# Kernel optimization log

Hardware: AMD Instinct MI355X
Metric: run time of the kernel (lower is better)

The kernel has to match this reference:

```python
import jax, jax.numpy as jnp
import numpy as np

D_MODEL = 1024
NUM_HEADS = 16
HEAD_DIM = D_MODEL // NUM_HEADS  # used only for score scaling, as in the torch code


def setup_inputs() -> dict:
    key = jax.random.key(0)
    ks = jax.random.split(key, 8)
    B, S, D = 4, 2048, D_MODEL
    w_scale = 1.0 / np.sqrt(D)
    return {
        "x": jax.random.normal(ks[0], (B, S, D), dtype=jnp.float32),
        "Wq": jax.random.normal(ks[1], (D, D), dtype=jnp.float32) * w_scale,
        "bq": jnp.zeros((D,), dtype=jnp.float32),
        "Wk": jax.random.normal(ks[2], (D, D), dtype=jnp.float32) * w_scale,
        "bk": jnp.zeros((D,), dtype=jnp.float32),
        "Wv": jax.random.normal(ks[3], (D, D), dtype=jnp.float32) * w_scale,
        "bv": jnp.zeros((D,), dtype=jnp.float32),
        "temperature_scale": jnp.ones((1,), dtype=jnp.float32),
    }


def reference(x, Wq, bq, Wk, bk, Wv, bv, temperature_scale):
    # q, k, v: (B, S, D) -- no head split in the original module
    q = x @ Wq + bq
    k = x @ Wk + bk
    v = x @ Wv + bv
    scale = jnp.asarray(HEAD_DIM, x.dtype) ** 0.5
    # scores: (B, S, S)
    scores = jnp.einsum("bqd,bkd->bqk", q, k) / scale / temperature_scale[0]
    probs = jax.nn.softmax(scores, axis=-1)
    # per-row attention entropy (B, S, 1)
    entropy = -jnp.sum(probs * jnp.log(probs + 1e-8), axis=-1, keepdims=True)
    attention_output = jnp.einsum("bqk,bkd->bqd", probs, v)
    return attention_output, entropy.mean()
```

## Files before the change

kernel.cpp:

```cpp
#include <hip/hip_runtime.h>
#include <hip/hip_bf16.h>
#include <cstdint>
#include <cstddef>


typedef __attribute__((ext_vector_type(8))) short short8;
typedef __attribute__((ext_vector_type(4))) short short4v;
typedef __attribute__((ext_vector_type(4))) float f32x4;

#define GLOBAL_AS __attribute__((address_space(1)))
#define LDS_AS __attribute__((address_space(3)))

__device__ __forceinline__ void async_load16(const void* g, void* lds) {
  __builtin_amdgcn_global_load_lds((GLOBAL_AS void*)g, (LDS_AS void*)lds, 16, 0, 0);
}

__device__ __forceinline__ short f2bf_s(float x) {
  __hip_bfloat16 h = __float2bfloat16(x);
  return *reinterpret_cast<short*>(&h);
}

template <int MODE>
__device__ __forceinline__
void gemm_body(const __hip_bfloat16* __restrict__ A,
               const __hip_bfloat16* __restrict__ Bt,
               void* __restrict__ Cout,
               const float* __restrict__ bias,
               int K, int lda, int ldb, int ldc,
               __hip_bfloat16* __restrict__ sA,
               __hip_bfloat16* __restrict__ sB,
               int m0, int n0,
               const float* __restrict__ aux) {
  const int tid  = threadIdx.x;
  const int lane = tid & 63;
  const int wid  = tid >> 6;
  const int wm = (wid >> 1) * 64;
  const int wn = (wid & 1) * 64;
  const int quad = lane >> 4;
  const int rc   = lane & 15;

  f32x4 acc[4][4] = {};

  const int srow = tid >> 3;
  const int scol = ((tid & 7) ^ ((tid >> 3) & 7)) * 8;
  const __hip_bfloat16* Ag = A  + (size_t)(m0 + srow) * lda + scol;
  const __hip_bfloat16* Bg = Bt + (size_t)(n0 + srow) * ldb + scol;

  for (int k0 = 0; k0 < K; k0 += 64) {
#pragma unroll
    for (int p = 0; p < 4; ++p) {
      async_load16(Ag + k0 + (size_t)(32 * p) * lda, &sA[(wid * 64 + 256 * p) * 8]);
      async_load16(Bg + k0 + (size_t)(32 * p) * ldb, &sB[(wid * 64 + 256 * p) * 8]);
    }
    __syncthreads();

#pragma unroll
    for (int kk = 0; kk < 2; ++kk) {
      const int xo = ((kk * 4 + quad) ^ (rc & 7)) * 8;
      short8 af[4], bf[4];
#pragma unroll
      for (int i = 0; i < 4; ++i)
        af[i] = *(const short8*)&sA[(wm + i * 16 + rc) * 64 + xo];
#pragma unroll
      for (int i = 0; i < 4; ++i)
        bf[i] = *(const short8*)&sB[(wn + i * 16 + rc) * 64 + xo];

#pragma unroll
      for (int mi = 0; mi < 4; ++mi)
#pragma unroll
        for (int ni = 0; ni < 4; ++ni)
          acc[mi][ni] = __builtin_amdgcn_mfma_f32_16x16x32_bf16(
              af[mi], bf[ni], acc[mi][ni], 0, 0, 0);
    }
    __syncthreads();
  }

  if (MODE == 4) {
#pragma unroll
    for (int mi = 0; mi < 4; ++mi) {
      float sc[4];
#pragma unroll
      for (int r = 0; r < 4; ++r)
        sc[r] = aux[m0 + wm + mi * 16 + quad * 4 + r];
#pragma unroll
      for (int ni = 0; ni < 4; ++ni) {
        const int col = n0 + wn + ni * 16 + rc;
#pragma unroll
        for (int r = 0; r < 4; ++r) {
          const int row = m0 + wm + mi * 16 + quad * 4 + r;
          ((float*)Cout)[(size_t)row * ldc + col] = acc[mi][ni][r] * sc[r];
        }
      }
    }
  } else {
    const float qsc = (MODE == 1 && aux) ? 1.0f / (8.0f * aux[0]) : 1.0f;
#pragma unroll
    for (int mi = 0; mi < 4; ++mi) {
#pragma unroll
      for (int ni = 0; ni < 4; ++ni) {
        const int col = n0 + wn + ni * 16 + rc;
        const float badd = bias[col];
        if (MODE == 2) {
          const int rowb = m0 + wm + mi * 16 + quad * 4;
          short4v o;
#pragma unroll
          for (int r = 0; r < 4; ++r) o[r] = f2bf_s(acc[mi][ni][r] + badd);
          const size_t idx = (size_t)(rowb >> 11) * (1024u * 2048u) +
                             (size_t)col * 2048u + (size_t)(rowb & 2047);
          *(short4v*)((short*)Cout + idx) = o;
        } else {
#pragma unroll
          for (int r = 0; r < 4; ++r) {
            const int row = m0 + wm + mi * 16 + quad * 4 + r;
            ((__hip_bfloat16*)Cout)[(size_t)row * ldc + col] =
                __float2bfloat16((acc[mi][ni][r] + badd) * qsc);
          }
        }
      }
    }
  }
}

__global__ __launch_bounds__(256)
void qkv_fused(const __hip_bfloat16* __restrict__ xb,
               const __hip_bfloat16* __restrict__ Wt,
               __hip_bfloat16* __restrict__ qb, __hip_bfloat16* __restrict__ kb,
               __hip_bfloat16* __restrict__ vt,
               const float* __restrict__ bq, const float* __restrict__ bk,
               const float* __restrict__ bv, const float* __restrict__ tptr) {
  __shared__ __align__(16) __hip_bfloat16 sA[128 * 64];
  __shared__ __align__(16) __hip_bfloat16 sB[128 * 64];
  const int lin = blockIdx.x;
  const int j = lin & 7, t = lin >> 3;
  const int x = t & 7;
  const int G = j + 8 * (t >> 3);
  const int z = G >> 6, y = G & 63;
  const int m0 = y * 128, n0 = x * 128;

  const __hip_bfloat16* B = Wt + (size_t)z * 1024 * 1024;
  if (z == 0)
    gemm_body<1>(xb, B, qb, bq, 1024, 1024, 1024, 1024, sA, sB, m0, n0, tptr);
  else if (z == 1)
    gemm_body<1>(xb, B, kb, bk, 1024, 1024, 1024, 1024, sA, sB, m0, n0, nullptr);
  else
    gemm_body<2>(xb, B, vt, bv, 1024, 1024, 1024, 0, sA, sB, m0, n0, nullptr);
}

__global__ __launch_bounds__(512)
void scores_bigm(const __hip_bfloat16* __restrict__ qb,
                 const __hip_bfloat16* __restrict__ kb,
                 __hip_bfloat16* __restrict__ Pt,
                 float* __restrict__ stats) {
  __shared__ __align__(16) __hip_bfloat16 sA[256 * 64];
  __shared__ __align__(16) __hip_bfloat16 sB[128 * 64];
  const int lin = blockIdx.x;
  const int G = (lin & 7) * 64 + (lin >> 3);
  const size_t z = G >> 7;
  const int rr = G & 127;
  const int y = rr >> 4;
  const int x = rr & 15;
  const int m0 = y * 256, n0 = x * 128;
  const __hip_bfloat16* A  = qb + z * 2048 * 1024;
  const __hip_bfloat16* Bt = kb + z * 2048 * 1024;
  __hip_bfloat16* Cout = Pt + z * 2048 * 2048;
  float* st = stats + z * 2048 * 64;

  const int tid  = threadIdx.x;
  const int lane = tid & 63;
  const int wid  = tid >> 6;
  const int wm   = (wid >> 1) * 64;
  const int wn   = (wid & 1) * 64;
  const int quad = lane >> 4;
  const int rc   = lane & 15;

  f32x4 acc[4][4] = {};

  const int srow = tid >> 3;
  const int scol = ((tid & 7) ^ ((tid >> 3) & 7)) * 8;
  const __hip_bfloat16* Ag = A  + (size_t)(m0 + srow) * 1024 + scol;
  const __hip_bfloat16* Bg = Bt + (size_t)(n0 + srow) * 1024 + scol;

  for (int k0 = 0; k0 < 1024; k0 += 64) {
#pragma unroll
    for (int p = 0; p < 4; ++p)
      async_load16(Ag + k0 + (size_t)(64 * p) * 1024, &sA[(tid + 512 * p) * 8]);
#pragma unroll
    for (int p = 0; p < 2; ++p)
      async_load16(Bg + k0 + (size_t)(64 * p) * 1024, &sB[(tid + 512 * p) * 8]);
    __syncthreads();

#pragma unroll
    for (int kk = 0; kk < 2; ++kk) {
      const int xo = ((kk * 4 + quad) ^ (rc & 7)) * 8;
      short8 af[4], bf[4];
#pragma unroll
      for (int i = 0; i < 4; ++i)
        af[i] = *(const short8*)&sA[(wm + i * 16 + rc) * 64 + xo];
#pragma unroll
      for (int i = 0; i < 4; ++i)
        bf[i] = *(const short8*)&sB[(wn + i * 16 + rc) * 64 + xo];

#pragma unroll
      for (int mi = 0; mi < 4; ++mi)
#pragma unroll
        for (int ni = 0; ni < 4; ++ni)
          acc[mi][ni] = __builtin_amdgcn_mfma_f32_16x16x32_bf16(
              af[mi], bf[ni], acc[mi][ni], 0, 0, 0);
    }
    __syncthreads();
  }

  const int chunk = (n0 + wn) >> 6;
#pragma unroll
  for (int mi = 0; mi < 4; ++mi) {
    float l_acc[4] = {}, w_acc[4] = {};
#pragma unroll
    for (int ni = 0; ni < 4; ++ni)
#pragma unroll
      for (int r = 0; r < 4; ++r) {
        const float xv = acc[mi][ni][r];
        const float e = __expf(xv);
        acc[mi][ni][r] = e;
        l_acc[r] += e;
        w_acc[r] += e * xv;
      }
#pragma unroll
    for (int r = 0; r < 4; ++r) {
      float l = l_acc[r], w = w_acc[r];
#pragma unroll
      for (int off = 1; off < 16; off <<= 1) {
        l += __shfl_xor(l, off);
        w += __shfl_xor(w, off);
      }
      if (rc == 0) {
        const int row = m0 + wm + mi * 16 + quad * 4 + r;
        *(float2*)&st[((size_t)row * 32 + chunk) * 2] = make_float2(l, w);
      }
    }
#pragma unroll
    for (int ni = 0; ni < 4; ++ni) {
      const int col = n0 + wn + ni * 16 + rc;
#pragma unroll
      for (int r = 0; r < 4; ++r) {
        const int row = m0 + wm + mi * 16 + quad * 4 + r;
        Cout[(size_t)row * 2048 + col] = __float2bfloat16(acc[mi][ni][r]);
      }
    }
  }
}

__global__ __launch_bounds__(256)
void pv_swz(const __hip_bfloat16* __restrict__ Pt,
            const __hip_bfloat16* __restrict__ vt,
            float* __restrict__ out,
            const float* __restrict__ inv_l) {
  __shared__ __align__(16) __hip_bfloat16 sA[128 * 64];
  __shared__ __align__(16) __hip_bfloat16 sB[128 * 64];
  const int lin = blockIdx.x;
  const int j = lin & 7, t = lin >> 3;
  const int w = t & 3;
  const int G = j + 8 * (t >> 2);
  const size_t z = G >> 5;
  const int r = G & 31;
  const int y = (r >> 2) * 2 + (w >> 1);
  const int x = (r & 3) * 2 + (w & 1);
  gemm_body<4>(Pt + z * 2048 * 2048, vt + z * 1024 * 2048,
               out + z * 2048 * 1024, nullptr, 2048, 2048, 2048, 1024,
               sA, sB, y * 128, x * 128, inv_l + z * 2048);
}

__global__ __launch_bounds__(256)
void prep_fused(const float* __restrict__ x, __hip_bfloat16* __restrict__ xb,
                const float* __restrict__ Wq, const float* __restrict__ Wk,
                const float* __restrict__ Wv, __hip_bfloat16* __restrict__ Wt) {
  if (blockIdx.x < 4096) {
    const int i = (blockIdx.x * 256 + threadIdx.x) * 8;
    const float4 a = *(const float4*)(x + i);
    const float4 b = *(const float4*)(x + i + 4);
    short8 o;
    o[0] = f2bf_s(a.x); o[1] = f2bf_s(a.y); o[2] = f2bf_s(a.z); o[3] = f2bf_s(a.w);
    o[4] = f2bf_s(b.x); o[5] = f2bf_s(b.y); o[6] = f2bf_s(b.z); o[7] = f2bf_s(b.w);
    *(short8*)((short*)xb + i) = o;
  } else {
    __shared__ float tile[64][65];
    const int b = blockIdx.x - 4096;
    const int z = b >> 8;
    const int rem = b & 255;
    const int c0 = (rem & 15) * 64;
    const int r0 = (rem >> 4) * 64;
    const float* src = (z == 0) ? Wq : (z == 1) ? Wk : Wv;
    __hip_bfloat16* dst = Wt + (size_t)z * 1024 * 1024;
    const int lane = threadIdx.x & 63;
    const int grp  = threadIdx.x >> 6;
#pragma unroll
    for (int i = 0; i < 16; ++i) {
      const int r = grp * 16 + i;
      tile[r][lane] = src[(size_t)(r0 + r) * 1024 + c0 + lane];
    }
    __syncthreads();
#pragma unroll
    for (int i = 0; i < 16; ++i) {
      const int r = grp * 16 + i;
      dst[(size_t)(c0 + r) * 1024 + r0 + lane] = __float2bfloat16(tile[lane][r]);
    }
  }
}

__global__ __launch_bounds__(256)
void stats_reduce(const float* __restrict__ stats,
                  float* __restrict__ inv_l, float* __restrict__ Hrow) {
  const int row = blockIdx.x * 256 + threadIdx.x;
  const float* sp = stats + (size_t)row * 64;
  float l = 0.f, w = 0.f;
#pragma unroll
  for (int j = 0; j < 16; ++j) {
    const float4 a = *(const float4*)(sp + j * 4);
    l += a.x + a.z;
    w += a.y + a.w;
  }
  const float il = 1.0f / l;
  inv_l[row] = il;
  Hrow[row] = __logf(l) - w * il;
}

__global__ __launch_bounds__(256)
void reduce_entropy(const float* __restrict__ Hrow, float* __restrict__ out) {
  const int tid  = threadIdx.x;
  const int lane = tid & 63;
  const int wid  = tid >> 6;
  float s = 0.f;
#pragma unroll
  for (int j = 0; j < 8; ++j) {
    const float4 a = *(const float4*)(Hrow + j * 1024 + tid * 4);
    s += a.x + a.y + a.z + a.w;
  }
#pragma unroll
  for (int off = 1; off < 64; off <<= 1) s += __shfl_xor(s, off);
  __shared__ float red[4];
  if (lane == 0) red[wid] = s;
  __syncthreads();
  if (tid == 0)
    out[0] = (red[0] + red[1] + red[2] + red[3]) * (1.0f / 8192.0f);
}

extern "C" void kernel_launch(void* const* d_in, const int* in_sizes, int n_in,
                              void* d_out, int out_size, void* d_ws, size_t ws_size,
                              hipStream_t stream) {
  const float* x    = (const float*)d_in[0];
  const float* Wq   = (const float*)d_in[1];
  const float* bq   = (const float*)d_in[2];
  const float* Wk   = (const float*)d_in[3];
  const float* bk   = (const float*)d_in[4];
  const float* Wv   = (const float*)d_in[5];
  const float* bv   = (const float*)d_in[6];
  const float* temp = (const float*)d_in[7];
  float* out = (float*)d_out;
  char* ws = (char*)d_ws;

  __hip_bfloat16* qb    = (__hip_bfloat16*)(ws + 0);
  __hip_bfloat16* kb    = (__hip_bfloat16*)(ws + 16777216);
  __hip_bfloat16* vt    = (__hip_bfloat16*)(ws + 33554432);
  __hip_bfloat16* xb    = (__hip_bfloat16*)(ws + 50331648);
  __hip_bfloat16* Wt    = (__hip_bfloat16*)(ws + 67108864);
  __hip_bfloat16* Pt    = (__hip_bfloat16*)(ws + 73400320);
  float*          stats = (float*)(ws + 106954752);
  float*          inv_l = (float*)(ws + 109051904);
  float*          Hrow  = (float*)(ws + 109084672);

  prep_fused<<<4864, 256, 0, stream>>>(x, xb, Wq, Wk, Wv, Wt);

  qkv_fused<<<1536, 256, 0, stream>>>(xb, Wt, qb, kb, vt, bq, bk, bv, temp);

  scores_bigm<<<512, 512, 0, stream>>>(qb, kb, Pt, stats);
  stats_reduce<<<32, 256, 0, stream>>>(stats, inv_l, Hrow);
  pv_swz<<<512, 256, 0, stream>>>(Pt, vt, out, inv_l);

  reduce_entropy<<<1, 256, 0, stream>>>(Hrow, out + 8388608);
}
```

Baseline: 242.1 us.

## Use 128x256 output tiles with 8 waves for the P·V GEMM

Replaces the 128x128, 256-thread P·V kernel with a dedicated 512-thread kernel that computes 128x256 tiles, so each loaded P tile is reused across twice as many output columns and the A-operand traffic drops. The grid is halved to 256 blocks, with a new XCD-aware block-to-tile mapping. The MODE 4 epilogue is removed from the shared GEMM body. The cost is a larger LDS footprint per block and only 256 blocks, one per CU, which may reduce latency hiding.

Result: slower. 247.1 us (+2.0%).

```diff
diff --git a/kernel.cpp b/kernel.cpp
--- a/kernel.cpp
+++ b/kernel.cpp
@@ -75,46 +75,27 @@
     __syncthreads();
   }
 
-  if (MODE == 4) {
-#pragma unroll
-    for (int mi = 0; mi < 4; ++mi) {
-      float sc[4];
-#pragma unroll
-      for (int r = 0; r < 4; ++r)
-        sc[r] = aux[m0 + wm + mi * 16 + quad * 4 + r];
-#pragma unroll
-      for (int ni = 0; ni < 4; ++ni) {
-        const int col = n0 + wn + ni * 16 + rc;
+  const float qsc = (MODE == 1 && aux) ? 1.0f / (8.0f * aux[0]) : 1.0f;
+#pragma unroll
+  for (int mi = 0; mi < 4; ++mi) {
+#pragma unroll
+    for (int ni = 0; ni < 4; ++ni) {
+      const int col = n0 + wn + ni * 16 + rc;
+      const float badd = bias[col];
+      if (MODE == 2) {
+        const int rowb = m0 + wm + mi * 16 + quad * 4;
+        short4v o;
+#pragma unroll
+        for (int r = 0; r < 4; ++r) o[r] = f2bf_s(acc[mi][ni][r] + badd);
+        const size_t idx = (size_t)(rowb >> 11) * (1024u * 2048u) +
+                           (size_t)col * 2048u + (size_t)(rowb & 2047);
+        *(short4v*)((short*)Cout + idx) = o;
+      } else {
 #pragma unroll
         for (int r = 0; r < 4; ++r) {
           const int row = m0 + wm + mi * 16 + quad * 4 + r;
-          ((float*)Cout)[(size_t)row * ldc + col] = acc[mi][ni][r] * sc[r];
-        }
-      }
-    }
-  } else {
-    const float qsc = (MODE == 1 && aux) ? 1.0f / (8.0f * aux[0]) : 1.0f;
-#pragma unroll
-    for (int mi = 0; mi < 4; ++mi) {
-#pragma unroll
-      for (int ni = 0; ni < 4; ++ni) {
-        const int col = n0 + wn + ni * 16 + rc;
-        const float badd = bias[col];
-        if (MODE == 2) {
-          const int rowb = m0 + wm + mi * 16 + quad * 4;
-          short4v o;
-#pragma unroll
-          for (int r = 0; r < 4; ++r) o[r] = f2bf_s(acc[mi][ni][r] + badd);
-          const size_t idx = (size_t)(rowb >> 11) * (1024u * 2048u) +
-                             (size_t)col * 2048u + (size_t)(rowb & 2047);
-          *(short4v*)((short*)Cout + idx) = o;
-        } else {
-#pragma unroll
-          for (int r = 0; r < 4; ++r) {
-            const int row = m0 + wm + mi * 16 + quad * 4 + r;
-            ((__hip_bfloat16*)Cout)[(size_t)row * ldc + col] =
-                __float2bfloat16((acc[mi][ni][r] + badd) * qsc);
-          }
+          ((__hip_bfloat16*)Cout)[(size_t)row * ldc + col] =
+              __float2bfloat16((acc[mi][ni][r] + badd) * qsc);
         }
       }
     }
@@ -249,24 +230,86 @@
   }
 }
 
-__global__ __launch_bounds__(256)
-void pv_swz(const __hip_bfloat16* __restrict__ Pt,
-            const __hip_bfloat16* __restrict__ vt,
-            float* __restrict__ out,
-            const float* __restrict__ inv_l) {
+__global__ __launch_bounds__(512)
+void pv_bign(const __hip_bfloat16* __restrict__ Pt,
+             const __hip_bfloat16* __restrict__ vt,
+             float* __restrict__ out,
+             const float* __restrict__ inv_l) {
   __shared__ __align__(16) __hip_bfloat16 sA[128 * 64];
-  __shared__ __align__(16) __hip_bfloat16 sB[128 * 64];
+  __shared__ __align__(16) __hip_bfloat16 sB[256 * 64];
   const int lin = blockIdx.x;
-  const int j = lin & 7, t = lin >> 3;
-  const int w = t & 3;
-  const int G = j + 8 * (t >> 2);
-  const size_t z = G >> 5;
-  const int r = G & 31;
-  const int y = (r >> 2) * 2 + (w >> 1);
-  const int x = (r & 3) * 2 + (w & 1);
-  gemm_body<4>(Pt + z * 2048 * 2048, vt + z * 1024 * 2048,
-               out + z * 2048 * 1024, nullptr, 2048, 2048, 2048, 1024,
-               sA, sB, y * 128, x * 128, inv_l + z * 2048);
+  const int G = (lin & 7) * 32 + (lin >> 3);
+  const size_t z = G >> 6;
+  const int rr = G & 63;
+  const int y = rr >> 2;
+  const int x = rr & 3;
+  const int m0 = y * 128, n0 = x * 256;
+  const __hip_bfloat16* A  = Pt + z * 2048 * 2048;
+  const __hip_bfloat16* Bt = vt + z * 1024 * 2048;
+  float* Cout = out + z * 2048 * 1024;
+  const float* il = inv_l + z * 2048;
+
+  const int tid  = threadIdx.x;
+  const int lane = tid & 63;
+  const int wid  = tid >> 6;
+  const int wm   = (wid >> 2) * 64;
+  const int wn   = (wid & 3) * 64;
+  const int quad = lane >> 4;
+  const int rc   = lane & 15;
+
+  f32x4 acc[4][4] = {};
+
+  const int srow = tid >> 3;
+  const int scol = ((tid & 7) ^ ((tid >> 3) & 7)) * 8;
+  const __hip_bfloat16* Ag = A  + (size_t)(m0 + srow) * 2048 + scol;
+  const __hip_bfloat16* Bg = Bt + (size_t)(n0 + srow) * 2048 + scol;
+
+  for (int k0 = 0; k0 < 2048; k0 += 64) {
+#pragma unroll
+    for (int p = 0; p < 2; ++p)
+      async_load16(Ag + k0 + (size_t)(64 * p) * 2048, &sA[(tid + 512 * p) * 8]);
+#pragma unroll
+    for (int p = 0; p < 4; ++p)
+      async_load16(Bg + k0 + (size_t)(64 * p) * 2048, &sB[(tid + 512 * p) * 8]);
+    __syncthreads();
+
+#pragma unroll
+    for (int kk = 0; kk < 2; ++kk) {
+      const int xo = ((kk * 4 + quad) ^ (rc & 7)) * 8;
+      short8 af[4], bf[4];
+#pragma unroll
+      for (int i = 0; i < 4; ++i)
+        af[i] = *(const short8*)&sA[(wm + i * 16 + rc) * 64 + xo];
+#pragma unroll
+      for (int i = 0; i < 4; ++i)
+        bf[i] = *(const short8*)&sB[(wn + i * 16 + rc) * 64 + xo];
+
+#pragma unroll
+      for (int mi = 0; mi < 4; ++mi)
+#pragma unroll
+        for (int ni = 0; ni < 4; ++ni)
+          acc[mi][ni] = __builtin_amdgcn_mfma_f32_16x16x32_bf16(
+              af[mi], bf[ni], acc[mi][ni], 0, 0, 0);
+    }
+    __syncthreads();
+  }
+
+#pragma unroll
+  for (int mi = 0; mi < 4; ++mi) {
+    float sc[4];
+#pragma unroll
+    for (int r = 0; r < 4; ++r)
+      sc[r] = il[m0 + wm + mi * 16 + quad * 4 + r];
+#pragma unroll
+    for (int ni = 0; ni < 4; ++ni) {
+      const int col = n0 + wn + ni * 16 + rc;
+#pragma unroll
+      for (int r = 0; r < 4; ++r) {
+        const int row = m0 + wm + mi * 16 + quad * 4 + r;
+        Cout[(size_t)row * 1024 + col] = acc[mi][ni][r] * sc[r];
+      }
+    }
+  }
 }
 
 __global__ __launch_bounds__(256)
@@ -373,7 +416,7 @@
 
   scores_bigm<<<512, 512, 0, stream>>>(qb, kb, Pt, stats);
   stats_reduce<<<32, 256, 0, stream>>>(stats, inv_l, Hrow);
-  pv_swz<<<512, 256, 0, stream>>>(Pt, vt, out, inv_l);
+  pv_bign<<<256, 512, 0, stream>>>(Pt, vt, out, inv_l);
 
   reduce_entropy<<<1, 256, 0, stream>>>(Hrow, out + 8388608);
 }
```
